# Kernel optimization log

Measured on AMD Instinct MI355X. Metric: run time of the kernel, lower is better.

## Reference

```python
import jax, jax.numpy as jnp
import numpy as np

DIM = 1024; HEADS = 16; DHEAD = 64; HID = 2048; E = 8; TOPK = 2
B = 2; S = 1024; SCTX = 1024
SCALE = DHEAD ** -0.5
INNER = HEADS * DHEAD


def setup_inputs() -> dict:
    key = jax.random.key(0)
    ks = jax.random.split(key, 20)
    w = lambda k, shape: jax.random.normal(k, shape, dtype=jnp.float32) * 0.02
    return {
        'x': jax.random.normal(ks[0], (B, S, DIM), dtype=jnp.float32),
        'enc_output': jax.random.normal(ks[1], (B, SCTX, DIM), dtype=jnp.float32),
        'src_mask': jnp.zeros((B, SCTX), dtype=bool),
        'tgt_mask': jax.random.randint(ks[2], (B, S), 0, 2).astype(bool),
        'tgt_mask_id_bool': jax.random.randint(ks[3], (B, S), 0, 2).astype(bool),
        'ln1_g': jnp.ones((DIM,), jnp.float32), 'ln1_b': jnp.zeros((DIM,), jnp.float32),
        'ln2_g': jnp.ones((DIM,), jnp.float32), 'ln2_b': jnp.zeros((DIM,), jnp.float32),
        'ln3_g': jnp.ones((DIM,), jnp.float32), 'ln3_b': jnp.zeros((DIM,), jnp.float32),
        'sa_wq': w(ks[4], (DIM, INNER)), 'sa_wk': w(ks[5], (DIM, INNER)),
        'sa_wv': w(ks[6], (DIM, INNER)), 'sa_wo': w(ks[7], (INNER, DIM)),
        'sa_bo': jnp.zeros((DIM,), jnp.float32),
        'ca_wq': w(ks[8], (DIM, INNER)), 'ca_wk': w(ks[9], (DIM, INNER)),
        'ca_wv': w(ks[10], (DIM, INNER)), 'ca_wo': w(ks[11], (INNER, DIM)),
        'ca_bo': jnp.zeros((DIM,), jnp.float32),
        'gate_w': w(ks[12], (DIM, E)),
        'cls_w': w(ks[13], (DIM, 1)), 'cls_b': jnp.zeros((1,), jnp.float32),
        'moe_w1': w(ks[14], (E, DIM, HID)),
        'moe_w2': w(ks[15], (E, HID, DIM)),
        'moe_w3': w(ks[16], (E, DIM, HID)),
    }


def layer_norm(x, g, b, eps=1e-5):
    m = jnp.mean(x, -1, keepdims=True)
    v = jnp.mean((x - m) ** 2, -1, keepdims=True)
    return (x - m) * jax.lax.rsqrt(v + eps) * g + b


def attention(x, ctx, mask, wq, wk, wv, wo, bo):
    b, n, _ = x.shape
    m = ctx.shape[1]
    q = (x @ wq).reshape(b, n, HEADS, DHEAD)
    k = (ctx @ wk).reshape(b, m, HEADS, DHEAD)
    v = (ctx @ wv).reshape(b, m, HEADS, DHEAD)
    sim = jnp.einsum('bihd,bjhd->bhij', q, k) * SCALE  # [b,h,n,m]
    sim = jnp.where(mask[:, None, None, :], jnp.finfo(sim.dtype).min, sim)
    attn = jax.nn.softmax(sim, axis=-1)
    out = jnp.einsum('bhij,bjhd->bihd', attn, v).reshape(b, n, INNER)
    return out @ wo + bo


def moe_ffn(x, tgt_pad, tgt_mid, gate_w, w1, w2, w3, cls_w, cls_b):
    b, s, d = x.shape
    xf = x.reshape(-1, d)                                   # [N, D]
    n = xf.shape[0]
    probs = jax.nn.softmax((xf @ gate_w).astype(jnp.float32), axis=-1)  # [N, E]
    router_probs = probs.reshape(b, s, E)
    topw, sel = jax.lax.top_k(probs, TOPK)                  # [N, k]
    topw = (topw / topw.sum(-1, keepdims=True)).astype(x.dtype)
    # dense token->expert weight matrix (0 for unselected experts)
    wtok = jnp.zeros((n, E), x.dtype).at[jnp.arange(n)[:, None], sel].set(topw)
    # SwiGLU experts computed densely, masked by routing weights
    h = jax.nn.silu(jnp.einsum('nd,edh->enh', xf, w1)) * jnp.einsum('nd,edh->enh', xf, w3)
    contrib = jnp.einsum('enh,ehd->end', h, w2) * wtok.T[:, :, None]    # [E, N, D]
    cum = jnp.cumsum(contrib, axis=0)                       # state after each expert's index_add_
    final = cum[-1].reshape(b, s, d)
    keep = (~(tgt_mid | tgt_pad)).astype(x.dtype)           # [b, s], 1 = non-padding
    denom = jnp.maximum(keep.sum(1), 1.0)                   # [b]
    emb = jnp.einsum('ebsd,bs->ebd', cum.reshape(E, b, s, d), keep) / denom[None, :, None]
    logits = emb @ cls_w + cls_b                            # [E, b, 1]
    return final, logits, router_probs


def reference(x, enc_output, src_mask, tgt_mask, tgt_mask_id_bool,
              ln1_g, ln1_b, ln2_g, ln2_b, ln3_g, ln3_b,
              sa_wq, sa_wk, sa_wv, sa_wo, sa_bo,
              ca_wq, ca_wk, ca_wv, ca_wo, ca_bo,
              gate_w, cls_w, cls_b, moe_w1, moe_w2, moe_w3):
    # self attention + residual + norm1
    attn_out = attention(x, x, tgt_mask, sa_wq, sa_wk, sa_wv, sa_wo, sa_bo)
    x = layer_norm(x + attn_out, ln1_g, ln1_b)
    # cross attention with encoder output + residual + norm2
    attn_out = attention(x, enc_output, src_mask, ca_wq, ca_wk, ca_wv, ca_wo, ca_bo)
    x = layer_norm(x + attn_out, ln2_g, ln2_b)
    # MoE feed forward + residual + norm3
    ff_out, expert_logits, router_probs = moe_ffn(
        x, tgt_mask, tgt_mask_id_bool, gate_w, moe_w1, moe_w2, moe_w3, cls_w, cls_b)
    x = layer_norm(x + ff_out, ln3_g, ln3_b)
    return x, expert_logits, router_probs
```

## Files before the change

kernel.cpp:

```cpp
#include <hip/hip_runtime.h>
#include <hip/hip_bf16.h>
#include <math.h>

constexpr int kB   = 2;
constexpr int kS   = 1024;
constexpr int kD   = 1024;
constexpr int kH   = 16;
constexpr int kDH  = 64;
constexpr int kHID = 2048;
constexpr int kE   = 8;
constexpr int kTok = kB * kS;
constexpr float kScale = 0.125f;
constexpr long long kOutLogits = (long long)kTok * kD;
constexpr long long kOutProbs  = kOutLogits + kE * kB;

using u16 = unsigned short;
typedef __attribute__((ext_vector_type(8))) short short8;
typedef __attribute__((ext_vector_type(4))) float f32x4;

__device__ __forceinline__ float b2f(u16 u) {
  union { unsigned int i; float f; } c; c.i = ((unsigned int)u) << 16; return c.f;
}
__device__ __forceinline__ u16 f2b(float f) {
  __hip_bfloat16 h = __float2bfloat16(f);
  u16 u; __builtin_memcpy(&u, &h, 2); return u;
}
__device__ __forceinline__ float ldIn(const void* p, long long i, int f32) {
  return f32 ? ((const float*)p)[i] : b2f(((const u16*)p)[i]);
}
__device__ __forceinline__ void ld8f(const void* p, long long i, int f32, float v[8]) {
  if (f32) {
    const float* fp = (const float*)p + i;
    float4 a = *(const float4*)fp, b = *(const float4*)(fp + 4);
    v[0]=a.x; v[1]=a.y; v[2]=a.z; v[3]=a.w; v[4]=b.x; v[5]=b.y; v[6]=b.z; v[7]=b.w;
  } else {
    short8 s = *(const short8*)((const u16*)p + i);
#pragma unroll
    for (int j = 0; j < 8; j++) v[j] = b2f((u16)s[j]);
  }
}
__device__ __forceinline__ void stOut(void* base, long long i, float v, int f32) {
  if (f32) ((float*)base)[i] = v; else ((u16*)base)[i] = f2b(v);
}

__device__ __forceinline__ void gll16(const void* g, void* l) {
  __builtin_amdgcn_global_load_lds(
      (__attribute__((address_space(1))) unsigned int*)(unsigned long long)g,
      (__attribute__((address_space(3))) unsigned int*)l, 16, 0, 0);
}

__device__ __forceinline__ float blockReduceSum(float v) {
  __shared__ float sh[4];
  int lane = threadIdx.x & 63, wv = threadIdx.x >> 6;
#pragma unroll
  for (int o = 32; o; o >>= 1) v += __shfl_down(v, o, 64);
  __syncthreads();
  if (lane == 0) sh[wv] = v;
  __syncthreads();
  return sh[0] + sh[1] + sh[2] + sh[3];
}
__device__ __forceinline__ float blockReduceMax(float v) {
  __shared__ float sh[4];
  int lane = threadIdx.x & 63, wv = threadIdx.x >> 6;
#pragma unroll
  for (int o = 32; o; o >>= 1) v = fmaxf(v, __shfl_down(v, o, 64));
  __syncthreads();
  if (lane == 0) sh[wv] = v;
  __syncthreads();
  return fmaxf(fmaxf(sh[0], sh[1]), fmaxf(sh[2], sh[3]));
}

__global__ void detect_k(const void* x, int* dflag) {
  __shared__ int sg, st;
  int tid = threadIdx.x;
  if (tid == 0) { sg = 0; st = 0; }
  __syncthreads();
  const unsigned int* w = (const unsigned int*)x;
  int good = 0, tot = 0;
  for (int i = tid; i < 1024; i += 256) {
    unsigned int lo = w[i] & 0xffffu;
    if (lo) {
      tot++;
      unsigned int e = (lo >> 7) & 0xffu;
      if (e >= 97 && e <= 159) good++;
    }
  }
  atomicAdd(&sg, good); atomicAdd(&st, tot);
  __syncthreads();
  if (tid == 0) dflag[0] = (sg * 10 < st * 9) ? 1 : 0;
}

__device__ __forceinline__ int key8(int r) { return (r ^ (r >> 3)) & 7; }

__global__ __launch_bounds__(256) void fattn_k(const u16* Qh, const u16* Ql,
                                               const u16* Kh, const u16* Kl,
                                               const u16* Vh, const u16* Vl,
                                               const float* maskf,
                                               u16* Oh, u16* Ol) {
  const int qt = blockIdx.x, bh = blockIdx.y;
  const int b = bh >> 4, hoff = (bh & 15) * 64;
  const int tid = threadIdx.x, wave = tid >> 6, lane = tid & 63;
  const int quad = lane >> 4, l16 = lane & 15, l7 = lane & 7;

  __shared__ __align__(16) u16 Ksh[64][64], Ksl[64][64];
  __shared__ __align__(16) u16 Vth[64][64], Vtl[64][64];
  __shared__ __align__(16) u16 Ps[4][2][1024];

  const long long tok0 = (long long)b * kS;
  const long long q0 = tok0 + qt * 64;

  short8 qh[2], qlo[2];
  {
    const long long qoff = (q0 + wave * 16 + l16) * kD + hoff;
#pragma unroll
    for (int kt = 0; kt < 2; kt++) {
      qh[kt]  = *(const short8*)(Qh + qoff + kt * 32 + quad * 8);
      qlo[kt] = *(const short8*)(Ql + qoff + kt * 32 + quad * 8);
    }
  }

  const int g0i = tid, g1i = 256 + tid;
  const int kr0 = g0i >> 3, kc0 = (g0i & 7) ^ key8(g0i >> 3);
  const int kr1 = g1i >> 3, kc1 = (g1i & 7) ^ key8(g1i >> 3);
  const int srow = tid >> 2, sd = (tid & 3) * 2;
  const int kvg = srow >> 3, kvo = srow & 7;

  f32x4 o[4];
  const f32x4 z4 = {0.f, 0.f, 0.f, 0.f};
  o[0] = z4; o[1] = z4; o[2] = z4; o[3] = z4;
  float mrow[4] = {-3e38f, -3e38f, -3e38f, -3e38f};
  float lrow[4] = {0.f, 0.f, 0.f, 0.f};

  short8 pk0, pk1, pk2, pk3;
  short8 pv0, pv1, pv2, pv3;

  auto loadRegs = [&](int t) {
    const long long kb0 = (tok0 + t * 64 + kr0) * kD + hoff + kc0 * 8;
    const long long kb1 = (tok0 + t * 64 + kr1) * kD + hoff + kc1 * 8;
    pk0 = *(const short8*)(Kh + kb0);
    pk1 = *(const short8*)(Kh + kb1);
    pk2 = *(const short8*)(Kl + kb0);
    pk3 = *(const short8*)(Kl + kb1);
    const long long vb = (tok0 + t * 64 + srow) * kD + hoff + sd * 8;
    pv0 = *(const short8*)(Vh + vb);
    pv1 = *(const short8*)(Vh + vb + 8);
    pv2 = *(const short8*)(Vl + vb);
    pv3 = *(const short8*)(Vl + vb + 8);
  };

  loadRegs(0);

#pragma unroll 1
  for (int t = 0; t < 16; t++) {
    if (t) __syncthreads();
    *(short8*)((u16*)Ksh + g0i * 8) = pk0;
    *(short8*)((u16*)Ksh + g1i * 8) = pk1;
    *(short8*)((u16*)Ksl + g0i * 8) = pk2;
    *(short8*)((u16*)Ksl + g1i * 8) = pk3;
#pragma unroll
    for (int j = 0; j < 16; j++) {
      const int d = sd * 8 + j;
      const int idx = ((kvg ^ key8(d)) << 3) + kvo;
      Vth[d][idx] = (u16)(j < 8 ? pv0[j] : pv1[j - 8]);
      Vtl[d][idx] = (u16)(j < 8 ? pv2[j] : pv3[j - 8]);
    }
    __syncthreads();
    if (t + 1 < 16) loadRegs(t + 1);
    f32x4 sa[4];
    sa[0] = z4; sa[1] = z4; sa[2] = z4; sa[3] = z4;
#pragma unroll
    for (int kt = 0; kt < 2; kt++) {
#pragma unroll
      for (int n = 0; n < 4; n++) {
        const int row = n * 16 + l16;
        const int g = (((kt * 4 + quad) ^ key8(row)) << 3);
        short8 bh = *(const short8*)&Ksh[row][g];
        short8 bl = *(const short8*)&Ksl[row][g];
        sa[n] = __builtin_amdgcn_mfma_f32_16x16x32_bf16(qlo[kt], bh, sa[n], 0, 0, 0);
        sa[n] = __builtin_amdgcn_mfma_f32_16x16x32_bf16(qh[kt], bl, sa[n], 0, 0, 0);
        sa[n] = __builtin_amdgcn_mfma_f32_16x16x32_bf16(qh[kt], bh, sa[n], 0, 0, 0);
      }
    }
    float s_[4][4];
    float pm[4] = {-3e38f, -3e38f, -3e38f, -3e38f};
#pragma unroll
    for (int n = 0; n < 4; n++) {
      const bool mb = maskf[b * kS + t * 64 + n * 16 + l16] != 0.f;
#pragma unroll
      for (int r = 0; r < 4; r++) {
        float v = mb ? -1e30f : sa[n][r] * kScale;
        s_[n][r] = v;
        pm[r] = fmaxf(pm[r], v);
      }
    }
#pragma unroll
    for (int mo = 1; mo < 16; mo <<= 1) {
#pragma unroll
      for (int r = 0; r < 4; r++) pm[r] = fmaxf(pm[r], __shfl_xor(pm[r], mo, 64));
    }
    float alpha[4], rs[4];
#pragma unroll
    for (int r = 0; r < 4; r++) {
      float mn = fmaxf(mrow[r], pm[r]);
      alpha[r] = __expf(mrow[r] - mn);
      mrow[r] = mn;
      rs[r] = 0.f;
    }
#pragma unroll
    for (int n = 0; n < 4; n++) {
#pragma unroll
      for (int r = 0; r < 4; r++) {
        float p = __expf(s_[n][r] - mrow[r]);
        s_[n][r] = p;
        rs[r] += p;
      }
    }
#pragma unroll
    for (int mo = 1; mo < 16; mo <<= 1) {
#pragma unroll
      for (int r = 0; r < 4; r++) rs[r] += __shfl_xor(rs[r], mo, 64);
    }
#pragma unroll
    for (int r = 0; r < 4; r++) {
      lrow[r] = lrow[r] * alpha[r] + rs[r];
#pragma unroll
      for (int n = 0; n < 4; n++) o[n][r] *= alpha[r];
    }
#pragma unroll
    for (int n = 0; n < 4; n++) {
      const int cg = n * 2 + (l16 >> 3);
#pragma unroll
      for (int r = 0; r < 4; r++) {
        const int row = quad * 4 + r;
        const int idx = row * 64 + ((cg ^ key8(row)) << 3) + l7;
        u16 hh = f2b(s_[n][r]);
        Ps[wave][0][idx] = hh;
        Ps[wave][1][idx] = f2b(s_[n][r] - b2f(hh));
      }
    }
    __syncthreads();
#pragma unroll
    for (int ks = 0; ks < 2; ks++) {
      const int gp = (((ks * 4 + quad) ^ key8(l16)) << 3);
      short8 ph = *(const short8*)&Ps[wave][0][l16 * 64 + gp];
      short8 pl = *(const short8*)&Ps[wave][1][l16 * 64 + gp];
#pragma unroll
      for (int n = 0; n < 4; n++) {
        const int row = n * 16 + l16;
        const int g = (((ks * 4 + quad) ^ key8(row)) << 3);
        short8 vh = *(const short8*)&Vth[row][g];
        short8 vl = *(const short8*)&Vtl[row][g];
        o[n] = __builtin_amdgcn_mfma_f32_16x16x32_bf16(pl, vh, o[n], 0, 0, 0);
        o[n] = __builtin_amdgcn_mfma_f32_16x16x32_bf16(ph, vl, o[n], 0, 0, 0);
        o[n] = __builtin_amdgcn_mfma_f32_16x16x32_bf16(ph, vh, o[n], 0, 0, 0);
      }
    }
  }
#pragma unroll
  for (int r = 0; r < 4; r++) {
    const float inv = 1.f / lrow[r];
    const long long ob = (q0 + wave * 16 + quad * 4 + r) * kD + hoff;
#pragma unroll
    for (int n = 0; n < 4; n++) {
      float val = o[n][r] * inv;
      u16 hh = f2b(val);
      Oh[ob + n * 16 + l16] = hh;
      Ol[ob + n * 16 + l16] = f2b(val - b2f(hh));
    }
  }
}

__global__ __launch_bounds__(256) void splitW_k(const void* s0, const void* s1, const void* s2,
                                                u16* h0, u16* l0, u16* h1, u16* l1,
                                                u16* h2, u16* l2, const int* dflag) {
  const int f32 = dflag[0];
  const void* src = blockIdx.z == 0 ? s0 : (blockIdx.z == 1 ? s1 : s2);
  u16* hi = blockIdx.z == 0 ? h0 : (blockIdx.z == 1 ? h1 : h2);
  u16* lo = blockIdx.z == 0 ? l0 : (blockIdx.z == 1 ? l1 : l2);
  const int gid = blockIdx.x * 256 + threadIdx.x;
  const int n = gid & 1023;
  const int kb8 = gid >> 10;
  const long long s0i = (long long)kb8 * 8 * 1024 + n;
  short8 h8, l8;
#pragma unroll
  for (int j = 0; j < 8; j++) {
    float v = ldIn(src, s0i + (long long)j * 1024, f32);
    u16 hh = f2b(v);
    h8[j] = (short)hh;
    l8[j] = (short)f2b(v - b2f(hh));
  }
  *(short8*)(hi + (long long)gid * 8) = h8;
  *(short8*)(lo + (long long)gid * 8) = l8;
}

__global__ __launch_bounds__(256) void splitA_k(const void* src, u16* hi, u16* lo,
                                                int forceF32, const int* dflag) {
  const int f32 = forceF32 ? 1 : dflag[0];
  const long long gid = (long long)blockIdx.x * 256 + threadIdx.x;
  float v[8];
  ld8f(src, gid * 8, f32, v);
  short8 h8, l8;
#pragma unroll
  for (int j = 0; j < 8; j++) {
    u16 hh = f2b(v[j]);
    h8[j] = (short)hh;
    l8[j] = (short)f2b(v[j] - b2f(hh));
  }
  *(short8*)(hi + gid * 8) = h8;
  *(short8*)(lo + gid * 8) = l8;
}

template <int NB, int OS>
__global__ __launch_bounds__(256) void gemmS_k(const u16* Ah, const u16* Al,
                                               const u16* Bh0, const u16* Bl0,
                                               const u16* Bh1, const u16* Bl1,
                                               const u16* Bh2, const u16* Bl2,
                                               void* C0, void* C1, void* C2,
                                               u16* Cl0, u16* Cl1, u16* Cl2,
                                               const void* bias, const int* dflag) {
  const int lin = blockIdx.y * gridDim.x + blockIdx.x;
  const int swz = (lin & 7) * 64 + (lin >> 3);
  const int tx = swz >> 5, ty = swz & 31;
  const int m0 = ty * 64, n0 = tx * 64;
  const int f32in = dflag[0];

  __shared__ __align__(16) u16 AhS[2][64][32], AlS[2][64][32];
  __shared__ __align__(16) u16 BhS[NB][2][4][64][8], BlS[NB][2][4][64][8];

  const int tid = threadIdx.x, wave = tid >> 6, lane = tid & 63;
  const int wr = wave >> 1, wc = wave & 1, quad = lane >> 4, l16 = lane & 15;

  const long long aOff = (long long)(m0 + (tid >> 2)) * kD + (tid & 3) * 8;
  const long long bOff = ((long long)(tid >> 6) * kD + n0 + (tid & 63)) * 8;
  const u16* pBh[3] = {Bh0, Bh1, Bh2};
  const u16* pBl[3] = {Bl0, Bl1, Bl2};
  void* pC[3] = {C0, C1, C2};
  u16* pCl[3] = {Cl0, Cl1, Cl2};

  f32x4 acc[NB][2][2];
  const f32x4 z4 = {0.f, 0.f, 0.f, 0.f};
#pragma unroll
  for (int i = 0; i < NB; i++) {
    acc[i][0][0] = z4; acc[i][0][1] = z4; acc[i][1][0] = z4; acc[i][1][1] = z4;
  }

  auto stage = [&](int buf, int kb) {
    gll16(Ah + aOff + kb * 32, (char*)&AhS[buf][0][0] + (wave << 10));
    gll16(Al + aOff + kb * 32, (char*)&AlS[buf][0][0] + (wave << 10));
    const long long bo = bOff + (long long)kb * (kD * 32);
#pragma unroll
    for (int i = 0; i < NB; i++) {
      gll16(pBh[i] + bo, (char*)&BhS[i][buf][0][0][0] + (wave << 10));
      gll16(pBl[i] + bo, (char*)&BlS[i][buf][0][0][0] + (wave << 10));
    }
  };

  stage(0, 0);
  __syncthreads();
  for (int kb = 0; kb < kD / 32; kb++) {
    const int cur = kb & 1;
    if (kb + 1 < kD / 32) stage(cur ^ 1, kb + 1);
    short8 ah0 = *(const short8*)&AhS[cur][wr * 32 + l16][quad * 8];
    short8 ah1 = *(const short8*)&AhS[cur][wr * 32 + 16 + l16][quad * 8];
    short8 al0 = *(const short8*)&AlS[cur][wr * 32 + l16][quad * 8];
    short8 al1 = *(const short8*)&AlS[cur][wr * 32 + 16 + l16][quad * 8];
#pragma unroll
    for (int i = 0; i < NB; i++) {
      short8 bh0 = *(const short8*)&BhS[i][cur][quad][wc * 32 + l16][0];
      short8 bh1 = *(const short8*)&BhS[i][cur][quad][wc * 32 + 16 + l16][0];
      short8 bl0 = *(const short8*)&BlS[i][cur][quad][wc * 32 + l16][0];
      short8 bl1 = *(const short8*)&BlS[i][cur][quad][wc * 32 + 16 + l16][0];
      acc[i][0][0] = __builtin_amdgcn_mfma_f32_16x16x32_bf16(al0, bh0, acc[i][0][0], 0, 0, 0);
      acc[i][0][1] = __builtin_amdgcn_mfma_f32_16x16x32_bf16(al0, bh1, acc[i][0][1], 0, 0, 0);
      acc[i][1][0] = __builtin_amdgcn_mfma_f32_16x16x32_bf16(al1, bh0, acc[i][1][0], 0, 0, 0);
      acc[i][1][1] = __builtin_amdgcn_mfma_f32_16x16x32_bf16(al1, bh1, acc[i][1][1], 0, 0, 0);
      acc[i][0][0] = __builtin_amdgcn_mfma_f32_16x16x32_bf16(ah0, bl0, acc[i][0][0], 0, 0, 0);
      acc[i][0][1] = __builtin_amdgcn_mfma_f32_16x16x32_bf16(ah0, bl1, acc[i][0][1], 0, 0, 0);
      acc[i][1][0] = __builtin_amdgcn_mfma_f32_16x16x32_bf16(ah1, bl0, acc[i][1][0], 0, 0, 0);
      acc[i][1][1] = __builtin_amdgcn_mfma_f32_16x16x32_bf16(ah1, bl1, acc[i][1][1], 0, 0, 0);
      acc[i][0][0] = __builtin_amdgcn_mfma_f32_16x16x32_bf16(ah0, bh0, acc[i][0][0], 0, 0, 0);
      acc[i][0][1] = __builtin_amdgcn_mfma_f32_16x16x32_bf16(ah0, bh1, acc[i][0][1], 0, 0, 0);
      acc[i][1][0] = __builtin_amdgcn_mfma_f32_16x16x32_bf16(ah1, bh0, acc[i][1][0], 0, 0, 0);
      acc[i][1][1] = __builtin_amdgcn_mfma_f32_16x16x32_bf16(ah1, bh1, acc[i][1][1], 0, 0, 0);
    }
    __syncthreads();
  }

#pragma unroll
  for (int i = 0; i < NB; i++) {
#pragma unroll
    for (int sm = 0; sm < 2; sm++) {
#pragma unroll
      for (int r = 0; r < 4; r++) {
        int row = m0 + wr * 32 + sm * 16 + quad * 4 + r;
#pragma unroll
        for (int sn = 0; sn < 2; sn++) {
          int col = n0 + wc * 32 + sn * 16 + l16;
          float v = acc[i][sm][sn][r];
          const long long idx = (long long)row * kD + col;
          if (OS) {
            u16 hh = f2b(v);
            ((u16*)pC[i])[idx] = hh;
            pCl[i][idx] = f2b(v - b2f(hh));
          } else {
            if (bias && i == 0) v += ldIn(bias, col, f32in);
            ((float*)pC[i])[idx] = v;
          }
        }
      }
    }
  }
}

__global__ __launch_bounds__(256) void cvtW_k(const void* src, u16* dst,
                                              int nSh, int kbSh, const int* dflag) {
  const int f32 = dflag[0];
  const int gid = blockIdx.x * 256 + threadIdx.x;
  const int N = 1 << nSh;
  const int n = gid & (N - 1);
  const int rest = gid >> nSh;
  const int kg = rest & 3;
  const int kb = (rest >> 2) & ((1 << kbSh) - 1);
  const int e = rest >> (2 + kbSh);
  const long long src0 = ((long long)e << (5 + kbSh + nSh)) +
                         (long long)(kb * 32 + kg * 8) * N + n;
  short8 o;
#pragma unroll
  for (int j = 0; j < 8; j++) o[j] = (short)f2b(ldIn(src, src0 + (long long)j * N, f32));
  *(short8*)(dst + (long long)gid * 8) = o;
}

__global__ __launch_bounds__(256) void cvtX_k(const float* src, u16* dst) {
  const int gid = blockIdx.x * 256 + threadIdx.x;
  const float* s = src + (long long)gid * 8;
  float4 a = *(const float4*)s, b = *(const float4*)(s + 4);
  short8 o;
  o[0]=(short)f2b(a.x); o[1]=(short)f2b(a.y); o[2]=(short)f2b(a.z); o[3]=(short)f2b(a.w);
  o[4]=(short)f2b(b.x); o[5]=(short)f2b(b.y); o[6]=(short)f2b(b.z); o[7]=(short)f2b(b.w);
  *(short8*)(dst + (long long)gid * 8) = o;
}

__global__ __launch_bounds__(256) void moe13_k(const u16* Xb, const u16* W1c, const u16* W3c,
                                               const int* counts, const int* offsets,
                                               const int* aidxArr, u16* Hbuf) {
  const int e = blockIdx.z;
  const int Meff = counts[e];
  const int m0 = blockIdx.y * 64;
  if (m0 >= Meff) return;
  const int n0 = blockIdx.x * 128;
  const int csr = offsets[e];

  __shared__ __align__(16) u16 As[2][64][32];
  __shared__ __align__(16) u16 B1s[2][4][128][8];
  __shared__ __align__(16) u16 B3s[2][4][128][8];

  const int tid = threadIdx.x, wave = tid >> 6, lane = tid & 63;
  const int wc = wave, quad = lane >> 4, l16 = lane & 15;

  int grow = m0 + (tid >> 2); if (grow >= Meff) grow = Meff - 1;
  const u16* pA = Xb + (long long)aidxArr[csr + grow] * kD + (tid & 3) * 8;

  const long long ebase = (long long)e * kD * kHID;
  const int g0 = tid, g1 = 256 + tid;
  const long long b0o = ebase + ((long long)(g0 >> 7) * kHID + n0 + (g0 & 127)) * 8;
  const long long b1o = ebase + ((long long)(g1 >> 7) * kHID + n0 + (g1 & 127)) * 8;

  f32x4 acc1[4][2], acc3[4][2];
  const f32x4 z4 = {0.f, 0.f, 0.f, 0.f};
#pragma unroll
  for (int i = 0; i < 4; i++) { acc1[i][0]=z4; acc1[i][1]=z4; acc3[i][0]=z4; acc3[i][1]=z4; }

  auto stage = [&](int buf, int kb) {
    gll16(pA + kb * 32, (char*)&As[buf][0][0] + (wave << 10));
    const long long ko = (long long)kb * (4 * kHID * 8);
    gll16(W1c + b0o + ko, (char*)&B1s[buf][0][0][0] + (wave << 10));
    gll16(W1c + b1o + ko, (char*)&B1s[buf][0][0][0] + 4096 + (wave << 10));
    gll16(W3c + b0o + ko, (char*)&B3s[buf][0][0][0] + (wave << 10));
    gll16(W3c + b1o + ko, (char*)&B3s[buf][0][0][0] + 4096 + (wave << 10));
  };

  stage(0, 0);
  __syncthreads();
  for (int kb = 0; kb < kD / 32; kb++) {
    const int cur = kb & 1;
    if (kb + 1 < kD / 32) stage(cur ^ 1, kb + 1);
    short8 af[4];
#pragma unroll
    for (int sm = 0; sm < 4; sm++)
      af[sm] = *(const short8*)&As[cur][sm * 16 + l16][quad * 8];
    short8 b1f[2], b3f[2];
#pragma unroll
    for (int sn = 0; sn < 2; sn++) {
      b1f[sn] = *(const short8*)&B1s[cur][quad][wc * 32 + sn * 16 + l16][0];
      b3f[sn] = *(const short8*)&B3s[cur][quad][wc * 32 + sn * 16 + l16][0];
    }
#pragma unroll
    for (int sm = 0; sm < 4; sm++) {
#pragma unroll
      for (int sn = 0; sn < 2; sn++) {
        acc1[sm][sn] = __builtin_amdgcn_mfma_f32_16x16x32_bf16(af[sm], b1f[sn], acc1[sm][sn], 0, 0, 0);
        acc3[sm][sn] = __builtin_amdgcn_mfma_f32_16x16x32_bf16(af[sm], b3f[sn], acc3[sm][sn], 0, 0, 0);
      }
    }
    __syncthreads();
  }

#pragma unroll
  for (int sm = 0; sm < 4; sm++) {
#pragma unroll
    for (int r = 0; r < 4; r++) {
      int row = m0 + sm * 16 + quad * 4 + r;
      if (row >= Meff) continue;
#pragma unroll
      for (int sn = 0; sn < 2; sn++) {
        int col = n0 + wc * 32 + sn * 16 + l16;
        float g1 = acc1[sm][sn][r], g3 = acc3[sm][sn][r];
        float h = (g1 / (1.f + __expf(-g1))) * g3;
        Hbuf[(long long)(csr + row) * kHID + col] = f2b(h);
      }
    }
  }
}

__global__ __launch_bounds__(256) void w2_k(const u16* Hbuf, const u16* W2c,
                                            const int* counts, const int* offsets,
                                            const int* aidxArr, const int* slotArr,
                                            const float* wgtArr, float* contrib) {
  const int e = blockIdx.z;
  const int Meff = counts[e];
  const int m0 = blockIdx.y * 64;
  if (m0 >= Meff) return;
  const int n0 = blockIdx.x * 128;
  const int csr = offsets[e];

  __shared__ __align__(16) u16 As[2][64][32];
  __shared__ __align__(16) u16 Bs[2][4][128][8];

  const int tid = threadIdx.x, wave = tid >> 6, lane = tid & 63;
  const int wc = wave, quad = lane >> 4, l16 = lane & 15;

  int grow = m0 + (tid >> 2); if (grow >= Meff) grow = Meff - 1;
  const u16* pA = Hbuf + (long long)(csr + grow) * kHID + (tid & 3) * 8;

  const long long ebase = (long long)e * kHID * kD;
  const int g0 = tid, g1 = 256 + tid;
  const long long b0o = ebase + ((long long)(g0 >> 7) * kD + n0 + (g0 & 127)) * 8;
  const long long b1o = ebase + ((long long)(g1 >> 7) * kD + n0 + (g1 & 127)) * 8;

  f32x4 acc[4][2];
  const f32x4 z4 = {0.f, 0.f, 0.f, 0.f};
#pragma unroll
  for (int i = 0; i < 4; i++) { acc[i][0] = z4; acc[i][1] = z4; }

  auto stage = [&](int buf, int kb) {
    gll16(pA + kb * 32, (char*)&As[buf][0][0] + (wave << 10));
    const long long ko = (long long)kb * (4 * kD * 8);
    gll16(W2c + b0o + ko, (char*)&Bs[buf][0][0][0] + (wave << 10));
    gll16(W2c + b1o + ko, (char*)&Bs[buf][0][0][0] + 4096 + (wave << 10));
  };

  stage(0, 0);
  __syncthreads();
  for (int kb = 0; kb < kHID / 32; kb++) {
    const int cur = kb & 1;
    if (kb + 1 < kHID / 32) stage(cur ^ 1, kb + 1);
    short8 af[4];
#pragma unroll
    for (int sm = 0; sm < 4; sm++)
      af[sm] = *(const short8*)&As[cur][sm * 16 + l16][quad * 8];
    short8 bf[2];
#pragma unroll
    for (int sn = 0; sn < 2; sn++)
      bf[sn] = *(const short8*)&Bs[cur][quad][wc * 32 + sn * 16 + l16][0];
#pragma unroll
    for (int sm = 0; sm < 4; sm++) {
#pragma unroll
      for (int sn = 0; sn < 2; sn++)
        acc[sm][sn] = __builtin_amdgcn_mfma_f32_16x16x32_bf16(af[sm], bf[sn], acc[sm][sn], 0, 0, 0);
    }
    __syncthreads();
  }

#pragma unroll
  for (int sm = 0; sm < 4; sm++) {
#pragma unroll
    for (int r = 0; r < 4; r++) {
      int row = m0 + sm * 16 + quad * 4 + r;
      if (row >= Meff) continue;
      int a = csr + row;
      int t = aidxArr[a]; int s = slotArr[a]; float w = wgtArr[a];
#pragma unroll
      for (int sn = 0; sn < 2; sn++) {
        int col = n0 + wc * 32 + sn * 16 + l16;
        contrib[((long long)s * kTok + t) * kD + col] = acc[sm][sn][r] * w;
      }
    }
  }
}

__global__ void maskprep_k(const void* srcm, const void* tgtm, const void* midm,
                           float* srcf, float* padf, float* keepf, float* denom) {
  __shared__ int okInt, okFloat, okBf16;
  int tid = threadIdx.x;
  if (tid == 0) { okInt = 1; okFloat = 1; okBf16 = 1; }
  __syncthreads();
  const unsigned int* wi = (const unsigned int*)tgtm;
  const float* wf = (const float*)tgtm;
  int badI = 0, badF = 0, badB = 0;
  for (int i = tid; i < 512; i += 256) {
    unsigned int w = wi[i];
    if (w > 1u) badI = 1;
    float f = wf[i];
    if (!(f == 0.f || f == 1.f)) badF = 1;
    unsigned int lo = w & 0xffffu, hi = w >> 16;
    if (!((lo == 0 || lo == 0x3f80u) && (hi == 0 || hi == 0x3f80u))) badB = 1;
  }
  if (badI) atomicExch(&okInt, 0);
  if (badF) atomicExch(&okFloat, 0);
  if (badB) atomicExch(&okBf16, 0);
  __syncthreads();
  int mode = okInt ? 0 : (okFloat ? 2 : (okBf16 ? 3 : 1));
  for (int i = tid; i < kTok; i += 256) {
    bool sv, pv, mv;
    if (mode == 0) {
      sv = ((const int*)srcm)[i] != 0; pv = ((const int*)tgtm)[i] != 0; mv = ((const int*)midm)[i] != 0;
    } else if (mode == 2) {
      sv = ((const float*)srcm)[i] != 0.f; pv = ((const float*)tgtm)[i] != 0.f; mv = ((const float*)midm)[i] != 0.f;
    } else if (mode == 3) {
      sv = ((const u16*)srcm)[i] != 0; pv = ((const u16*)tgtm)[i] != 0; mv = ((const u16*)midm)[i] != 0;
    } else {
      sv = ((const unsigned char*)srcm)[i] != 0; pv = ((const unsigned char*)tgtm)[i] != 0; mv = ((const unsigned char*)midm)[i] != 0;
    }
    srcf[i] = sv ? 1.f : 0.f;
    padf[i] = pv ? 1.f : 0.f;
    keepf[i] = (pv || mv) ? 0.f : 1.f;
  }
  __syncthreads();
  if (tid < 2) {
    float s = 0;
    for (int j = 0; j < kS; j++) s += keepf[tid * kS + j];
    denom[tid] = fmaxf(s, 1.f);
  }
}

__global__ __launch_bounds__(256) void ln_k(const float* basef, const void* baseb,
                                            const int* dflag, int baseIsIn,
                                            const float* add1, const float* add2,
                                            const void* g, const void* bb,
                                            float* outf, void* outFinal) {
  const int f32in = dflag[0];
  const int baseF32 = baseIsIn && f32in;
  long long base = (long long)blockIdx.x * kD;
  int tid = threadIdx.x;
  float v[4]; float s = 0;
#pragma unroll
  for (int i = 0; i < 4; i++) {
    int d = tid + i * 256;
    float x = basef ? basef[base + d] : ldIn(baseb, base + d, baseF32);
    if (add1) x += add1[base + d];
    if (add2) x += add2[base + d];
    v[i] = x; s += x;
  }
  float mean = blockReduceSum(s) * (1.f / kD);
  float q = 0;
#pragma unroll
  for (int i = 0; i < 4; i++) { float d0 = v[i] - mean; q += d0 * d0; }
  float var = blockReduceSum(q) * (1.f / kD);
  float rstd = rsqrtf(var + 1e-5f);
#pragma unroll
  for (int i = 0; i < 4; i++) {
    int d = tid + i * 256;
    float y = (v[i] - mean) * rstd * ldIn(g, d, f32in) + ldIn(bb, d, f32in);
    if (outf) outf[base + d] = y;
    if (outFinal) stOut(outFinal, base + d, y, f32in);
  }
}

__global__ __launch_bounds__(256) void router_k(const float* xf, const void* gw, void* outBase,
                                                int* sel, float* wsel, int* counts,
                                                const int* dflag) {
  const int f32in = dflag[0];
  int wv = threadIdx.x >> 6, lane = threadIdx.x & 63;
  int t = blockIdx.x * 4 + wv;
  const float* xr = xf + (long long)t * kD;
  float acc[8];
#pragma unroll
  for (int e = 0; e < 8; e++) acc[e] = 0.f;
  for (int d = lane; d < kD; d += 64) {
    float xv = xr[d];
    float gv[8];
    ld8f(gw, (long long)d * 8, f32in, gv);
#pragma unroll
    for (int e = 0; e < 8; e++) acc[e] += xv * gv[e];
  }
#pragma unroll
  for (int o = 32; o; o >>= 1) {
#pragma unroll
    for (int e = 0; e < 8; e++) acc[e] += __shfl_down(acc[e], o, 64);
  }
  if (lane == 0) {
    float mx = acc[0];
    for (int e = 1; e < 8; e++) mx = fmaxf(mx, acc[e]);
    float p[8], sum = 0;
    for (int e = 0; e < 8; e++) { p[e] = expf(acc[e] - mx); sum += p[e]; }
    float inv = 1.f / sum;
    for (int e = 0; e < 8; e++) {
      p[e] *= inv;
      stOut(outBase, kOutProbs + (long long)t * 8 + e, p[e], f32in);
    }
    int e0 = 0; for (int e = 1; e < 8; e++) if (p[e] > p[e0]) e0 = e;
    int e1 = -1; for (int e = 0; e < 8; e++) { if (e == e0) continue; if (e1 < 0 || p[e] > p[e1]) e1 = e; }
    float s2 = p[e0] + p[e1];
    sel[t * 2] = e0; sel[t * 2 + 1] = e1;
    wsel[t * 2] = p[e0] / s2; wsel[t * 2 + 1] = p[e1] / s2;
    atomicAdd(&counts[e0], 1); atomicAdd(&counts[e1], 1);
  }
}

__global__ void offsets_k(const int* counts, int* offsets) {
  if (threadIdx.x == 0) {
    int s = 0;
    for (int e = 0; e < kE; e++) { offsets[e] = s; s += counts[e]; }
    offsets[kE] = s;
  }
}

__global__ void place_k(const int* sel, const float* wsel, const int* offsets, int* fill,
                        int* aidxArr, int* slotArr, float* wgtArr) {
  int t = blockIdx.x * 256 + threadIdx.x;
  if (t >= kTok) return;
  for (int s = 0; s < 2; s++) {
    int e = sel[t * 2 + s];
    int pos = offsets[e] + atomicAdd(&fill[e], 1);
    aidxArr[pos] = t; slotArr[pos] = s; wgtArr[pos] = wsel[t * 2 + s];
  }
}

__global__ void meanacc_k(const int* counts, const int* offsets, const int* aidxArr,
                          const int* slotArr, const float* keepf, const float* contrib,
                          float* meanAcc) {
  int e = blockIdx.x, dc = blockIdx.y, ch = blockIdx.z;
  int d = dc * 128 + threadIdx.x;
  int cnt = counts[e], off = offsets[e];
  int per = (cnt + 15) / 16;
  int i0 = ch * per, i1 = i0 + per; if (i1 > cnt) i1 = cnt;
  float a0 = 0, a1 = 0;
  for (int i = i0; i < i1; i++) {
    int a = off + i; int t = aidxArr[a];
    if (keepf[t] != 0.f) {
      float v = contrib[((long long)slotArr[a] * kTok + t) * kD + d];
      if (t < kS) a0 += v; else a1 += v;
    }
  }
  if (a0 != 0.f) atomicAdd(&meanAcc[(e * 2 + 0) * kD + d], a0);
  if (a1 != 0.f) atomicAdd(&meanAcc[(e * 2 + 1) * kD + d], a1);
}

__global__ __launch_bounds__(256) void dots_k(const float* meanAcc, const void* cls_w,
                                              const float* denom, float* dots,
                                              const int* dflag) {
  const int f32in = dflag[0];
  int eb = blockIdx.x;
  int b = eb & 1;
  float s = 0;
  for (int d = threadIdx.x; d < kD; d += 256)
    s += meanAcc[(long long)eb * kD + d] * ldIn(cls_w, d, f32in);
  s = blockReduceSum(s);
  if (threadIdx.x == 0) dots[eb] = s / denom[b];
}

__global__ void final_logits_k(const float* dots, const void* cls_b, void* outBase,
                               const int* dflag) {
  const int f32in = dflag[0];
  int i = threadIdx.x;
  if (i < kE * kB) {
    int e = i >> 1, b = i & 1;
    float s = ldIn(cls_b, 0, f32in);
    for (int e2 = 0; e2 <= e; e2++) s += dots[e2 * 2 + b];
    stOut(outBase, kOutLogits + e * kB + b, s, f32in);
  }
}

extern "C" void kernel_launch(void* const* d_in, const int* in_sizes, int n_in,
                              void* d_out, int out_size, void* d_ws, size_t ws_size,
                              hipStream_t stream) {
  (void)in_sizes; (void)n_in; (void)out_size; (void)ws_size;

  const void* x_in  = d_in[0];
  const void* enc   = d_in[1];
  const void* srcm = d_in[2];
  const void* tgtm = d_in[3];
  const void* midm = d_in[4];
  const void* ln1g = d_in[5];  const void* ln1b = d_in[6];
  const void* ln2g = d_in[7];  const void* ln2b = d_in[8];
  const void* ln3g = d_in[9];  const void* ln3b = d_in[10];
  const void* sa_wq = d_in[11]; const void* sa_wk = d_in[12];
  const void* sa_wv = d_in[13]; const void* sa_wo = d_in[14];
  const void* sa_bo = d_in[15];
  const void* ca_wq = d_in[16]; const void* ca_wk = d_in[17];
  const void* ca_wv = d_in[18]; const void* ca_wo = d_in[19];
  const void* ca_bo = d_in[20];
  const void* gate_w = d_in[21];
  const void* cls_w  = d_in[22]; const void* cls_b = d_in[23];
  const void* moe_w1 = d_in[24];
  const void* moe_w2 = d_in[25];
  const void* moe_w3 = d_in[26];

  char* wp = (char*)d_ws;
  size_t off = 0;
  auto alloc = [&](size_t bytes) -> void* {
    void* p = wp + off; off = (off + bytes + 255) & ~(size_t)255; return p;
  };
  float* scFP = (float*)alloc((size_t)16 * kS * kS * 4);
  u16*   Hbuf = (u16*)scFP;
  float* contrib = (float*)((char*)scFP + (size_t)2 * kTok * kHID * 2);
  float* qf    = (float*)alloc((size_t)kTok * kD * 4);
  float* kf    = (float*)alloc((size_t)kTok * kD * 4);
  float* vf    = (float*)alloc((size_t)kTok * kD * 4);
  float* attnof= (float*)alloc((size_t)kTok * kD * 4);
  float* obuf  = (float*)alloc((size_t)kTok * kD * 4);
  float* x1f   = (float*)alloc((size_t)kTok * kD * 4);
  float* x2f   = (float*)alloc((size_t)kTok * kD * 4);
  float* meanAcc = (float*)alloc((size_t)kE * kB * kD * 4);
  float* srcf = (float*)alloc(kTok * 4);
  float* padf = (float*)alloc(kTok * 4);
  float* keepf = (float*)alloc(kTok * 4);
  float* denom = (float*)alloc(2 * 4);
  int* counts = (int*)alloc(256); int* fill = counts + 8;
  int* offsets = (int*)alloc(256);
  int* sel = (int*)alloc(kTok * 2 * 4);
  float* wsel = (float*)alloc(kTok * 2 * 4);
  int* aidxArr = (int*)alloc(2 * kTok * 4);
  int* slotArr = (int*)alloc(2 * kTok * 4);
  float* wgtArr = (float*)alloc(2 * kTok * 4);
  float* dots = (float*)alloc(256);
  int* dflag = (int*)alloc(256);

  u16* WH0 = (u16*)x2f;
  u16* WL0 = WH0 + (1 << 20);
  u16* WH1 = WL0 + (1 << 20);
  u16* WL1 = WH1 + (1 << 20);
  u16* WH2 = (u16*)x1f;
  u16* WL2 = WH2 + (1 << 20);
  u16* AH  = (u16*)scFP;
  u16* AL  = AH + (2 << 20);

  u16* Qh = (u16*)qf;     u16* Ql = Qh + (2 << 20);
  u16* Kh = (u16*)kf;     u16* Kl = Kh + (2 << 20);
  u16* Vh = (u16*)vf;     u16* Vl = Vh + (2 << 20);
  u16* Oh = (u16*)attnof; u16* Ol = Oh + (2 << 20);

  u16* W1c = (u16*)qf;
  u16* W2c = (u16*)qf;
  u16* W3c = (u16*)((char*)scFP + ((size_t)32 << 20));
  u16* Xb  = (u16*)obuf;

  hipMemsetAsync(counts, 0, 64, stream);
  hipMemsetAsync(meanAcc, 0, (size_t)kE * kB * kD * 4, stream);
  detect_k<<<1, 256, 0, stream>>>(x_in, dflag);
  maskprep_k<<<1, 256, 0, stream>>>(srcm, tgtm, midm, srcf, padf, keepf, denom);

  const dim3 gGrid(16, 32);
  const dim3 aGrid(kS / 64, 32);

  splitA_k<<<1024, 256, 0, stream>>>(x_in, AH, AL, 0, dflag);
  splitW_k<<<dim3(512, 1, 3), 256, 0, stream>>>(sa_wq, sa_wk, sa_wv,
      WH0, WL0, WH1, WL1, WH2, WL2, dflag);
  gemmS_k<3, 1><<<gGrid, 256, 0, stream>>>(AH, AL, WH0, WL0, WH1, WL1, WH2, WL2,
      Qh, Kh, Vh, Ql, Kl, Vl, nullptr, dflag);
  fattn_k<<<aGrid, 256, 0, stream>>>(Qh, Ql, Kh, Kl, Vh, Vl, padf, Oh, Ol);
  splitW_k<<<dim3(512, 1, 1), 256, 0, stream>>>(sa_wo, nullptr, nullptr,
      WH0, WL0, nullptr, nullptr, nullptr, nullptr, dflag);
  gemmS_k<1, 0><<<gGrid, 256, 0, stream>>>(Oh, Ol, WH0, WL0, WH0, WL0, WH0, WL0,
      obuf, obuf, obuf, nullptr, nullptr, nullptr, sa_bo, dflag);
  ln_k<<<kTok, 256, 0, stream>>>(nullptr, x_in, dflag, 1, obuf, nullptr, ln1g, ln1b, x1f, nullptr);

  splitA_k<<<1024, 256, 0, stream>>>(x1f, AH, AL, 1, dflag);
  splitW_k<<<dim3(512, 1, 1), 256, 0, stream>>>(ca_wq, nullptr, nullptr,
      WH0, WL0, nullptr, nullptr, nullptr, nullptr, dflag);
  gemmS_k<1, 1><<<gGrid, 256, 0, stream>>>(AH, AL, WH0, WL0, WH0, WL0, WH0, WL0,
      Qh, Qh, Qh, Ql, Ql, Ql, nullptr, dflag);
  splitA_k<<<1024, 256, 0, stream>>>(enc, AH, AL, 0, dflag);
  splitW_k<<<dim3(512, 1, 2), 256, 0, stream>>>(ca_wk, ca_wv, nullptr,
      WH0, WL0, WH1, WL1, nullptr, nullptr, dflag);
  gemmS_k<2, 1><<<gGrid, 256, 0, stream>>>(AH, AL, WH0, WL0, WH1, WL1, WH0, WL0,
      Kh, Vh, Vh, Kl, Vl, Vl, nullptr, dflag);
  fattn_k<<<aGrid, 256, 0, stream>>>(Qh, Ql, Kh, Kl, Vh, Vl, srcf, Oh, Ol);
  splitW_k<<<dim3(512, 1, 1), 256, 0, stream>>>(ca_wo, nullptr, nullptr,
      WH0, WL0, nullptr, nullptr, nullptr, nullptr, dflag);
  gemmS_k<1, 0><<<gGrid, 256, 0, stream>>>(Oh, Ol, WH0, WL0, WH0, WL0, WH0, WL0,
      obuf, obuf, obuf, nullptr, nullptr, nullptr, ca_bo, dflag);
  ln_k<<<kTok, 256, 0, stream>>>(x1f, nullptr, dflag, 0, obuf, nullptr, ln2g, ln2b, x2f, nullptr);

  router_k<<<kTok / 4, 256, 0, stream>>>(x2f, gate_w, d_out, sel, wsel, counts, dflag);
  offsets_k<<<1, 64, 0, stream>>>(counts, offsets);
  place_k<<<kTok / 256, 256, 0, stream>>>(sel, wsel, offsets, fill, aidxArr, slotArr, wgtArr);

  cvtX_k<<<kTok * kD / (8 * 256), 256, 0, stream>>>(x2f, Xb);
  const int wGrid = (kE * kD * kHID / 8) / 256;
  cvtW_k<<<wGrid, 256, 0, stream>>>(moe_w1, W1c, 11, 5, dflag);
  cvtW_k<<<wGrid, 256, 0, stream>>>(moe_w3, W3c, 11, 5, dflag);

  moe13_k<<<dim3(kHID / 128, kTok / 64, kE), 256, 0, stream>>>(
      Xb, W1c, W3c, counts, offsets, aidxArr, Hbuf);

  cvtW_k<<<wGrid, 256, 0, stream>>>(moe_w2, W2c, 10, 6, dflag);

  w2_k<<<dim3(kD / 128, kTok / 64, kE), 256, 0, stream>>>(
      Hbuf, W2c, counts, offsets, aidxArr, slotArr, wgtArr, contrib);

  meanacc_k<<<dim3(kE, kD / 128, 16), 128, 0, stream>>>(counts, offsets, aidxArr, slotArr, keepf, contrib, meanAcc);
  dots_k<<<kE * kB, 256, 0, stream>>>(meanAcc, cls_w, denom, dots, dflag);
  final_logits_k<<<1, 64, 0, stream>>>(dots, cls_b, d_out, dflag);
  ln_k<<<kTok, 256, 0, stream>>>(x2f, nullptr, dflag, 0, contrib, contrib + (size_t)kTok * kD, ln3g, ln3b, nullptr, d_out);
}
```

Measured before the change: 899.5 us.

## Remap block indices for XCD locality and enlarge MoE gate/up tile to 128 rows

The flash-attention grid becomes 1D and is remapped so that blocks dispatched to the same XCD (round-robin by lin&7) share a few batch-heads and so reuse K/V in that XCD's L2. The GEMM block swizzle is changed so each XCD covers an 8x8 tile region, aiming for better A/B reuse in L2. The MoE W1/W3 kernel doubles its M tile to 128 rows with 512 threads and 8 waves, so each weight tile loaded into LDS serves twice as many tokens. The trade-offs are more shared memory per block, fewer blocks for experts with few tokens, and more wasted rows when an expert's token count is just over a multiple of 128.

Measured after the change: 880.6 us. 2.1% less time.

```diff
diff --git a/kernel.cpp b/kernel.cpp
--- a/kernel.cpp
+++ b/kernel.cpp
@@ -97,7 +97,10 @@
                                                const u16* Vh, const u16* Vl,
                                                const float* maskf,
                                                u16* Oh, u16* Ol) {
-  const int qt = blockIdx.x, bh = blockIdx.y;
+  const int lin = blockIdx.x;
+  const int xc = lin & 7, li = lin >> 3;
+  const int bh = xc * 4 + (li >> 4);
+  const int qt = li & 15;
   const int b = bh >> 4, hoff = (bh & 15) * 64;
   const int tid = threadIdx.x, wave = tid >> 6, lane = tid & 63;
   const int quad = lane >> 4, l16 = lane & 15, l7 = lane & 7;
@@ -174,11 +177,11 @@
       for (int n = 0; n < 4; n++) {
         const int row = n * 16 + l16;
         const int g = (((kt * 4 + quad) ^ key8(row)) << 3);
-        short8 bh = *(const short8*)&Ksh[row][g];
-        short8 bl = *(const short8*)&Ksl[row][g];
-        sa[n] = __builtin_amdgcn_mfma_f32_16x16x32_bf16(qlo[kt], bh, sa[n], 0, 0, 0);
-        sa[n] = __builtin_amdgcn_mfma_f32_16x16x32_bf16(qh[kt], bl, sa[n], 0, 0, 0);
-        sa[n] = __builtin_amdgcn_mfma_f32_16x16x32_bf16(qh[kt], bh, sa[n], 0, 0, 0);
+        short8 bh_ = *(const short8*)&Ksh[row][g];
+        short8 bl_ = *(const short8*)&Ksl[row][g];
+        sa[n] = __builtin_amdgcn_mfma_f32_16x16x32_bf16(qlo[kt], bh_, sa[n], 0, 0, 0);
+        sa[n] = __builtin_amdgcn_mfma_f32_16x16x32_bf16(qh[kt], bl_, sa[n], 0, 0, 0);
+        sa[n] = __builtin_amdgcn_mfma_f32_16x16x32_bf16(qh[kt], bh_, sa[n], 0, 0, 0);
       }
     }
     float s_[4][4];
@@ -319,8 +322,9 @@
                                                u16* Cl0, u16* Cl1, u16* Cl2,
                                                const void* bias, const int* dflag) {
   const int lin = blockIdx.y * gridDim.x + blockIdx.x;
-  const int swz = (lin & 7) * 64 + (lin >> 3);
-  const int tx = swz >> 5, ty = swz & 31;
+  const int xc = lin & 7, li = lin >> 3;
+  const int ty = (xc & 3) * 8 + (li >> 3);
+  const int tx = (xc >> 2) * 8 + (li & 7);
   const int m0 = ty * 64, n0 = tx * 64;
   const int f32in = dflag[0];
 
@@ -440,30 +444,28 @@
   *(short8*)(dst + (long long)gid * 8) = o;
 }
 
-__global__ __launch_bounds__(256) void moe13_k(const u16* Xb, const u16* W1c, const u16* W3c,
+__global__ __launch_bounds__(512) void moe13_k(const u16* Xb, const u16* W1c, const u16* W3c,
                                                const int* counts, const int* offsets,
                                                const int* aidxArr, u16* Hbuf) {
   const int e = blockIdx.z;
   const int Meff = counts[e];
-  const int m0 = blockIdx.y * 64;
+  const int m0 = blockIdx.y * 128;
   if (m0 >= Meff) return;
   const int n0 = blockIdx.x * 128;
   const int csr = offsets[e];
 
-  __shared__ __align__(16) u16 As[2][64][32];
+  __shared__ __align__(16) u16 As[2][128][32];
   __shared__ __align__(16) u16 B1s[2][4][128][8];
   __shared__ __align__(16) u16 B3s[2][4][128][8];
 
   const int tid = threadIdx.x, wave = tid >> 6, lane = tid & 63;
-  const int wc = wave, quad = lane >> 4, l16 = lane & 15;
+  const int wr = wave >> 2, wc = wave & 3, quad = lane >> 4, l16 = lane & 15;
 
   int grow = m0 + (tid >> 2); if (grow >= Meff) grow = Meff - 1;
   const u16* pA = Xb + (long long)aidxArr[csr + grow] * kD + (tid & 3) * 8;
 
   const long long ebase = (long long)e * kD * kHID;
-  const int g0 = tid, g1 = 256 + tid;
-  const long long b0o = ebase + ((long long)(g0 >> 7) * kHID + n0 + (g0 & 127)) * 8;
-  const long long b1o = ebase + ((long long)(g1 >> 7) * kHID + n0 + (g1 & 127)) * 8;
+  const long long bo = ebase + ((long long)(tid >> 7) * kHID + n0 + (tid & 127)) * 8;
 
   f32x4 acc1[4][2], acc3[4][2];
   const f32x4 z4 = {0.f, 0.f, 0.f, 0.f};
@@ -473,10 +475,8 @@
   auto stage = [&](int buf, int kb) {
     gll16(pA + kb * 32, (char*)&As[buf][0][0] + (wave << 10));
     const long long ko = (long long)kb * (4 * kHID * 8);
-    gll16(W1c + b0o + ko, (char*)&B1s[buf][0][0][0] + (wave << 10));
-    gll16(W1c + b1o + ko, (char*)&B1s[buf][0][0][0] + 4096 + (wave << 10));
-    gll16(W3c + b0o + ko, (char*)&B3s[buf][0][0][0] + (wave << 10));
-    gll16(W3c + b1o + ko, (char*)&B3s[buf][0][0][0] + 4096 + (wave << 10));
+    gll16(W1c + bo + ko, (char*)&B1s[buf][0][0][0] + (wave << 10));
+    gll16(W3c + bo + ko, (char*)&B3s[buf][0][0][0] + (wave << 10));
   };
 
   stage(0, 0);
@@ -487,7 +487,7 @@
     short8 af[4];
 #pragma unroll
     for (int sm = 0; sm < 4; sm++)
-      af[sm] = *(const short8*)&As[cur][sm * 16 + l16][quad * 8];
+      af[sm] = *(const short8*)&As[cur][wr * 64 + sm * 16 + l16][quad * 8];
     short8 b1f[2], b3f[2];
 #pragma unroll
     for (int sn = 0; sn < 2; sn++) {
@@ -509,7 +509,7 @@
   for (int sm = 0; sm < 4; sm++) {
 #pragma unroll
     for (int r = 0; r < 4; r++) {
-      int row = m0 + sm * 16 + quad * 4 + r;
+      int row = m0 + wr * 64 + sm * 16 + quad * 4 + r;
       if (row >= Meff) continue;
 #pragma unroll
       for (int sn = 0; sn < 2; sn++) {
@@ -861,7 +861,7 @@
   maskprep_k<<<1, 256, 0, stream>>>(srcm, tgtm, midm, srcf, padf, keepf, denom);
 
   const dim3 gGrid(16, 32);
-  const dim3 aGrid(kS / 64, 32);
+  const dim3 aGrid(512);
 
   splitA_k<<<1024, 256, 0, stream>>>(x_in, AH, AL, 0, dflag);
   splitW_k<<<dim3(512, 1, 3), 256, 0, stream>>>(sa_wq, sa_wk, sa_wv,
@@ -901,7 +901,7 @@
   cvtW_k<<<wGrid, 256, 0, stream>>>(moe_w1, W1c, 11, 5, dflag);
   cvtW_k<<<wGrid, 256, 0, stream>>>(moe_w3, W3c, 11, 5, dflag);
 
-  moe13_k<<<dim3(kHID / 128, kTok / 64, kE), 256, 0, stream>>>(
+  moe13_k<<<dim3(kHID / 128, kTok / 128, kE), 512, 0, stream>>>(
       Xb, W1c, W3c, counts, offsets, aidxArr, Hbuf);
 
   cvtW_k<<<wGrid, 256, 0, stream>>>(moe_w2, W2c, 10, 6, dflag);
```
